# Kernel tuning notes

Hardware: AMD Instinct MI355X
Metric: run time of the kernel (lower is better)

## Reference

```python
import jax, jax.numpy as jnp
import numpy as np

D_MODEL = 1024
H = 16
D_K = D_MODEL // H


def setup_inputs() -> dict:
    key = jax.random.key(0)
    ks = jax.random.split(key, 7)
    B, S = 4, 2048
    scale = 1.0 / np.sqrt(D_MODEL)
    return {
        "q": jax.random.normal(ks[0], (B, S, D_MODEL), dtype=jnp.float32),
        "k": jax.random.normal(ks[1], (B, S, D_MODEL), dtype=jnp.float32),
        "v": jax.random.normal(ks[2], (B, S, D_MODEL), dtype=jnp.float32),
        "W_q": jax.random.normal(ks[3], (D_MODEL, D_MODEL), dtype=jnp.float32) * scale,
        "W_k": jax.random.normal(ks[4], (D_MODEL, D_MODEL), dtype=jnp.float32) * scale,
        "W_v": jax.random.normal(ks[5], (D_MODEL, D_MODEL), dtype=jnp.float32) * scale,
        "W_o": jax.random.normal(ks[6], (D_MODEL, D_MODEL), dtype=jnp.float32) * scale,
    }


def reference(q, k, v, W_q, W_k, W_v, W_o):
    B, S, _ = q.shape
    # nn.Linear(bias=False): y = x @ W.T
    def proj(x, W):
        return (x @ W.T).reshape(B, -1, H, D_K).transpose(0, 2, 1, 3)  # [B,H,S,d_k]
    Q = proj(q, W_q)
    K = proj(k, W_k)
    V = proj(v, W_v)
    scores = jnp.einsum('bhqd,bhkd->bhqk', Q, K) / jnp.sqrt(jnp.float32(D_K))
    attn = jax.nn.softmax(scores, axis=-1)  # dropout p=0.0 -> identity
    ctx = jnp.einsum('bhqk,bhkd->bhqd', attn, V)
    ctx = ctx.transpose(0, 2, 1, 3).reshape(B, S, H * D_K)
    return ctx @ W_o.T
```

## Files before the change

### kernel.cpp

```cpp
#include <hip/hip_runtime.h>
#include <stdint.h>


typedef __attribute__((ext_vector_type(8))) short bf16x8;
typedef __attribute__((ext_vector_type(4))) float f32x4;

__device__ __forceinline__ void lds_async16(const void* g, void* l) {
  __builtin_amdgcn_global_load_lds(
      (const __attribute__((address_space(1))) void*)g,
      (__attribute__((address_space(3))) void*)l, 16, 0, 0);
}

__device__ __forceinline__ unsigned short f2bf(float f) {
  union { float f; unsigned u; } v; v.f = f;
  unsigned u = v.u + 0x7fffu + ((v.u >> 16) & 1u);
  return (unsigned short)(u >> 16);
}

__device__ __forceinline__ float fast_exp2(float x) {
#if __has_builtin(__builtin_amdgcn_exp2f)
  return __builtin_amdgcn_exp2f(x);
#else
  return exp2f(x);
#endif
}

__device__ __forceinline__ unsigned pk2(float a, float b) {
#if __has_builtin(__builtin_amdgcn_cvt_pk_bf16_f32)
  typedef __bf16 bf16v2 __attribute__((ext_vector_type(2)));
  union { bf16v2 v; unsigned u; } x;
  x.v = __builtin_amdgcn_cvt_pk_bf16_f32(a, b);
  return x.u;
#else
  return (unsigned)f2bf(a) | ((unsigned)f2bf(b) << 16);
#endif
}

__global__ void cvt_kernel(const float* s0, const float* s1, const float* s2, const float* s3,
                           unsigned short* d0, unsigned short* d1, unsigned short* d2, unsigned short* d3,
                           int n4) {
  int which = blockIdx.y;
  const float* s = which == 0 ? s0 : which == 1 ? s1 : which == 2 ? s2 : s3;
  unsigned short* d = which == 0 ? d0 : which == 1 ? d1 : which == 2 ? d2 : d3;
  int i = blockIdx.x * 256 + threadIdx.x;
  if (i < n4) {
    float4 v = ((const float4*)s)[i];
    ushort4 o;
    o.x = f2bf(v.x); o.y = f2bf(v.y); o.z = f2bf(v.z); o.w = f2bf(v.w);
    ((ushort4*)d)[i] = o;
  }
}

struct GemmAcc { f32x4 acc[4][4]; };

__device__ __forceinline__ void gemm_core(const unsigned short* __restrict__ Arows,
                                          const unsigned short* __restrict__ Brows,
                                          int tm, int tn, unsigned short* As,
                                          unsigned short* Bs, GemmAcc& g) {
  constexpr int K = 1024;
  const int tid = threadIdx.x;
  const int lane = tid & 63;
  const int wv = tid >> 6;
  const int wm = wv & 1, wn = wv >> 1;
  const int c16 = lane & 15, q4 = lane >> 4;

#pragma unroll
  for (int i = 0; i < 4; ++i)
#pragma unroll
    for (int j = 0; j < 4; ++j)
#pragma unroll
      for (int r = 0; r < 4; ++r) g.acc[i][j][r] = 0.f;

  const int srow = tid >> 3;
  const int gc = (((tid & 7) ^ (srow & 7)) << 3);
  const unsigned short* Arow = Arows + (size_t)(tm * 128 + srow) * K + gc;
  const unsigned short* Brow = Brows + (size_t)(tn * 128 + srow) * K + gc;
  char* AsBase = (char*)As + tid * 16;
  char* BsBase = (char*)Bs + tid * 16;

  for (int k0 = 0; k0 < K; k0 += 64) {
    __syncthreads();
#pragma unroll
    for (int i = 0; i < 4; ++i) {
      lds_async16(Arow + k0 + i * 32 * K, AsBase + i * 4096);
      lds_async16(Brow + k0 + i * 32 * K, BsBase + i * 4096);
    }
    __syncthreads();
#pragma unroll
    for (int ks = 0; ks < 2; ++ks) {
      bf16x8 af[4], bfr[4];
#pragma unroll
      for (int i = 0; i < 4; ++i) {
        int mr = wm * 64 + i * 16 + c16;
        int pa = (ks * 4 + q4) ^ (mr & 7);
        af[i] = *(const bf16x8*)(As + mr * 64 + pa * 8);
        int nr = wn * 64 + i * 16 + c16;
        int pb = (ks * 4 + q4) ^ (nr & 7);
        bfr[i] = *(const bf16x8*)(Bs + nr * 64 + pb * 8);
      }
#pragma unroll
      for (int i = 0; i < 4; ++i)
#pragma unroll
        for (int j = 0; j < 4; ++j)
          g.acc[i][j] = __builtin_amdgcn_mfma_f32_16x16x32_bf16(af[i], bfr[j], g.acc[i][j], 0, 0, 0);
    }
  }
}

__global__ __launch_bounds__(256, 2)
void qkv_kernel(const unsigned short* __restrict__ qb, const unsigned short* __restrict__ kb,
                const unsigned short* __restrict__ vb,
                const unsigned short* __restrict__ wq, const unsigned short* __restrict__ wk,
                const unsigned short* __restrict__ wv_,
                unsigned short* __restrict__ Qb, unsigned short* __restrict__ Kb,
                unsigned short* __restrict__ Vtb) {
  __shared__ unsigned short As[128 * 64];
  __shared__ unsigned short Bs[128 * 64];
  const int z = blockIdx.z;
  const unsigned short* A;
  const unsigned short* B;
  int tm, tn;
  if (z == 0)      { A = qb;  B = wq;  tm = blockIdx.y; tn = blockIdx.x; }
  else if (z == 1) { A = kb;  B = wk;  tm = blockIdx.y; tn = blockIdx.x; }
  else             { A = wv_; B = vb;  tm = blockIdx.x; tn = blockIdx.y; }

  GemmAcc g;
  gemm_core(A, B, tm, tn, As, Bs, g);

  const int lane = threadIdx.x & 63;
  const int wv = threadIdx.x >> 6;
  const int wm = wv & 1, wn = wv >> 1;
  const int c16 = lane & 15, q4 = lane >> 4;
  const float qscale = 0.125f * 1.44269504f;

#pragma unroll
  for (int i = 0; i < 4; ++i)
#pragma unroll
    for (int j = 0; j < 4; ++j)
#pragma unroll
      for (int r = 0; r < 4; ++r) {
        int m = tm * 128 + wm * 64 + i * 16 + q4 * 4 + r;
        int n = tn * 128 + wn * 64 + j * 16 + c16;
        float val = g.acc[i][j][r];
        if (z < 2) {
          if (z == 0) val *= qscale;
          int b = m >> 11, s_ = m & 2047, h = n >> 6, d = n & 63;
          unsigned short* dst = z == 0 ? Qb : Kb;
          dst[(((size_t)(b * 16 + h) * 2048 + s_) << 6) | d] = f2bf(val);
        } else {
          int h = m >> 6, d = m & 63, b = n >> 11, s_ = n & 2047;
          int sl = s_ & 127;
          int sp = (sl & ~31) | (((sl >> 2) & 3) << 3) | (((sl >> 4) & 1) << 2) | (sl & 3);
          s_ = (s_ & ~127) | sp;
          Vtb[((size_t)((b * 16 + h) * 64 + d) << 11) | s_] = f2bf(val);
        }
      }
}

__global__ __launch_bounds__(256, 2)
void out_gemm(const unsigned short* __restrict__ A, const unsigned short* __restrict__ B,
              float* __restrict__ C) {
  __shared__ unsigned short As[128 * 64];
  __shared__ unsigned short Bs[128 * 64];
  GemmAcc g;
  gemm_core(A, B, blockIdx.y, blockIdx.x, As, Bs, g);
  const int lane = threadIdx.x & 63;
  const int wv = threadIdx.x >> 6;
  const int wm = wv & 1, wn = wv >> 1;
  const int c16 = lane & 15, q4 = lane >> 4;
#pragma unroll
  for (int i = 0; i < 4; ++i)
#pragma unroll
    for (int j = 0; j < 4; ++j)
#pragma unroll
      for (int r = 0; r < 4; ++r) {
        int m = blockIdx.y * 128 + wm * 64 + i * 16 + q4 * 4 + r;
        int n = blockIdx.x * 128 + wn * 64 + j * 16 + c16;
        C[(size_t)m * 1024 + n] = g.acc[i][j][r];
      }
}

__global__ __launch_bounds__(256, 2)
void attn_kernel(const unsigned short* __restrict__ Q,
                 const unsigned short* __restrict__ K,
                 const unsigned short* __restrict__ Vt,
                 unsigned short* __restrict__ ctx) {
  __shared__ unsigned short Ks[2][128 * 64];
  __shared__ unsigned short Vs[2][64 * 128];

  const int tid = threadIdx.x, lane = tid & 63, w = tid >> 6;
  const int c16 = lane & 15, q4 = lane >> 4;
  const int wbase = w * 64;
  const int bh = blockIdx.y, qt = blockIdx.x;
  const unsigned short* Qp = Q + ((size_t)bh * 2048 + qt * 256) * 64;
  const unsigned short* Kp = K + (size_t)bh * 2048 * 64;
  const unsigned short* Vp = Vt + (size_t)bh * 64 * 2048;

  const int srow8 = tid >> 3;
  const int gc8 = (((tid & 7) ^ (srow8 & 7)) << 3);

  {
    const unsigned short* Qr = Qp + (size_t)srow8 * 64 + gc8;
    char* base = (char*)Ks + tid * 16;
#pragma unroll
    for (int c = 0; c < 8; ++c) lds_async16(Qr + c * 32 * 64, base + c * 4096);
  }
  __syncthreads();
  const unsigned short* Kflat = &Ks[0][0];
  bf16x8 qf[4][2];
#pragma unroll
  for (int nn = 0; nn < 4; ++nn)
#pragma unroll
    for (int ks = 0; ks < 2; ++ks) {
      int qr = wbase + nn * 16 + c16;
      int pos = (ks * 4 + q4) ^ (qr & 7);
      qf[nn][ks] = *(const bf16x8*)(Kflat + qr * 64 + pos * 8);
    }
  __syncthreads();

  bf16x8 onesf;
  {
    short v = (c16 == 0) ? (short)0x3F80 : (short)0;
#pragma unroll
    for (int j = 0; j < 8; ++j) onesf[j] = v;
  }

  f32x4 oacc[4][4];
  f32x4 lacc[4];
#pragma unroll
  for (int nn = 0; nn < 4; ++nn) {
#pragma unroll
    for (int r = 0; r < 4; ++r) lacc[nn][r] = 0.f;
#pragma unroll
    for (int dj = 0; dj < 4; ++dj)
#pragma unroll
      for (int r = 0; r < 4; ++r) oacc[nn][dj][r] = 0.f;
  }

  const int vrow = tid >> 4;
  const int vslot = tid & 15;
  const int vchunk = vslot ^ (vrow & 15);
  const unsigned short* Kr0 = Kp + (size_t)srow8 * 64 + gc8;
  const unsigned short* Vr0 = Vp + (size_t)vrow * 2048 + vchunk * 8;

  {
    char* kb = (char*)Ks[0] + tid * 16;
    char* vb = (char*)Vs[0] + tid * 16;
#pragma unroll
    for (int c = 0; c < 4; ++c) {
      lds_async16(Kr0 + c * 32 * 64, kb + c * 4096);
      lds_async16(Vr0 + (size_t)c * 16 * 2048, vb + c * 4096);
    }
  }

  int cur = 0;
  for (int kt = 0; kt < 16; ++kt) {
    __syncthreads();
    if (kt < 15) {
      char* kb = (char*)Ks[cur ^ 1] + tid * 16;
      char* vb = (char*)Vs[cur ^ 1] + tid * 16;
      const unsigned short* Krn = Kr0 + (size_t)(kt + 1) * 128 * 64;
      const unsigned short* Vrn = Vr0 + (size_t)(kt + 1) * 128;
#pragma unroll
      for (int c = 0; c < 4; ++c) {
        lds_async16(Krn + c * 32 * 64, kb + c * 4096);
        lds_async16(Vrn + (size_t)c * 16 * 2048, vb + c * 4096);
      }
    }

    const unsigned short* KsC = Ks[cur];
    const unsigned short* VsC = Vs[cur];

#pragma unroll
    for (int ks2 = 0; ks2 < 4; ++ks2) {
      f32x4 s[2][4];
#pragma unroll
      for (int ms = 0; ms < 2; ++ms) {
        const int row = (ks2 * 2 + ms) * 16 + c16;
        const bf16x8 kf0 = *(const bf16x8*)(KsC + row * 64 + ((0 + q4) ^ (row & 7)) * 8);
        const bf16x8 kf1 = *(const bf16x8*)(KsC + row * 64 + ((4 + q4) ^ (row & 7)) * 8);
#pragma unroll
        for (int nn = 0; nn < 4; ++nn) {
          f32x4 z = {0.f, 0.f, 0.f, 0.f};
          z = __builtin_amdgcn_mfma_f32_16x16x32_bf16(kf0, qf[nn][0], z, 0, 0, 0);
          z = __builtin_amdgcn_mfma_f32_16x16x32_bf16(kf1, qf[nn][1], z, 0, 0, 0);
          s[ms][nn] = z;
        }
      }
      bf16x8 pfv[4];
#pragma unroll
      for (int nn = 0; nn < 4; ++nn) {
        union PU { unsigned u[4]; bf16x8 v; } pf;
        pf.u[0] = pk2(fast_exp2(s[0][nn][0]), fast_exp2(s[0][nn][1]));
        pf.u[1] = pk2(fast_exp2(s[0][nn][2]), fast_exp2(s[0][nn][3]));
        pf.u[2] = pk2(fast_exp2(s[1][nn][0]), fast_exp2(s[1][nn][1]));
        pf.u[3] = pk2(fast_exp2(s[1][nn][2]), fast_exp2(s[1][nn][3]));
        pfv[nn] = pf.v;
        lacc[nn] = __builtin_amdgcn_mfma_f32_16x16x32_bf16(pf.v, onesf, lacc[nn], 0, 0, 0);
      }
#pragma unroll
      for (int dj = 0; dj < 4; ++dj) {
        const int dr = dj * 16 + c16;
        const bf16x8 vf = *(const bf16x8*)(VsC + dr * 128 + (((ks2 * 4 + q4) ^ (dr & 15))) * 8);
#pragma unroll
        for (int nn = 0; nn < 4; ++nn)
          oacc[nn][dj] = __builtin_amdgcn_mfma_f32_16x16x32_bf16(pfv[nn], vf, oacc[nn][dj], 0, 0, 0);
      }
    }
    cur ^= 1;
  }

  int b = bh >> 4, h = bh & 15;
#pragma unroll
  for (int nn = 0; nn < 4; ++nn)
#pragma unroll
    for (int r = 0; r < 4; ++r) {
      float l = __shfl(lacc[nn][r], lane & 48, 64);
      float inv = 1.f / l;
      int s_ = qt * 256 + wbase + nn * 16 + q4 * 4 + r;
#pragma unroll
      for (int dj = 0; dj < 4; ++dj) {
        int d = dj * 16 + c16;
        ctx[((size_t)(b * 2048 + s_)) * 1024 + h * 64 + d] = f2bf(oacc[nn][dj][r] * inv);
      }
    }
}

extern "C" void kernel_launch(void* const* d_in, const int* in_sizes, int n_in,
                              void* d_out, int out_size, void* d_ws, size_t ws_size,
                              hipStream_t stream) {
  const float* q  = (const float*)d_in[0];
  const float* k  = (const float*)d_in[1];
  const float* v  = (const float*)d_in[2];
  const float* Wq = (const float*)d_in[3];
  const float* Wk = (const float*)d_in[4];
  const float* Wv = (const float*)d_in[5];
  const float* Wo = (const float*)d_in[6];

  char* ws = (char*)d_ws;
  unsigned short* qb  = (unsigned short*)(ws);
  unsigned short* kb  = (unsigned short*)(ws + (16u << 20));
  unsigned short* vb  = (unsigned short*)(ws + (32u << 20));
  unsigned short* wqb = (unsigned short*)(ws + (48u << 20));
  unsigned short* wkb = (unsigned short*)(ws + (50u << 20));
  unsigned short* wvb = (unsigned short*)(ws + (52u << 20));
  unsigned short* wob = (unsigned short*)(ws + (54u << 20));
  unsigned short* Qb  = (unsigned short*)(ws + (56u << 20));
  unsigned short* Kb  = (unsigned short*)(ws + (72u << 20));
  unsigned short* Vtb = (unsigned short*)(ws + (88u << 20));
  unsigned short* ctxb = qb;

  cvt_kernel<<<dim3(1024, 4), 256, 0, stream>>>(Wq, Wk, Wv, Wo, wqb, wkb, wvb, wob, 262144);
  cvt_kernel<<<dim3(8192, 3), 256, 0, stream>>>(q, k, v, q, qb, kb, vb, qb, 2097152);

  qkv_kernel<<<dim3(8, 64, 3), 256, 0, stream>>>(qb, kb, vb, wqb, wkb, wvb, Qb, Kb, Vtb);

  attn_kernel<<<dim3(8, 64), 256, 0, stream>>>(Qb, Kb, Vtb, ctxb);

  out_gemm<<<dim3(8, 64), 256, 0, stream>>>(ctxb, wob, (float*)d_out);
}
```

Before: 331.6 us.

## Shrink attention blocks to two waves with 64-key tiles, remapped grid and setprio

The attention kernel now runs 128-thread blocks over 128 query rows with 64-key K/V tiles, so it launches 1024 smaller workgroups on a 1D grid. The grid index is remapped so neighbouring workgroups handle different batch-heads. V fragment loads are hoisted ahead of the exp step, and s_setprio raises wave priority around the MFMA sections to encourage overlap between waves. The aim is more resident workgroups and better MFMA/VALU interleaving, at the cost of twice as many loop iterations and barriers, and K/V being loaded by twice as many blocks per head.

```diff
diff --git a/kernel.cpp b/kernel.cpp
--- a/kernel.cpp
+++ b/kernel.cpp
@@ -180,30 +180,32 @@
       }
 }
 
-__global__ __launch_bounds__(256, 2)
+__global__ __launch_bounds__(128, 2)
 void attn_kernel(const unsigned short* __restrict__ Q,
                  const unsigned short* __restrict__ K,
                  const unsigned short* __restrict__ Vt,
                  unsigned short* __restrict__ ctx) {
-  __shared__ unsigned short Ks[2][128 * 64];
-  __shared__ unsigned short Vs[2][64 * 128];
+  __shared__ unsigned short Ks[2][64 * 64];
+  __shared__ unsigned short Vs[2][64 * 64];
 
   const int tid = threadIdx.x, lane = tid & 63, w = tid >> 6;
   const int c16 = lane & 15, q4 = lane >> 4;
   const int wbase = w * 64;
-  const int bh = blockIdx.y, qt = blockIdx.x;
-  const unsigned short* Qp = Q + ((size_t)bh * 2048 + qt * 256) * 64;
+  const unsigned wgid = blockIdx.x;
+  const int bh = (int)((wgid & 7u) * 8 + ((wgid >> 3) & 7u));
+  const int qt = (int)(wgid >> 6);
+  const unsigned short* Qp = Q + ((size_t)bh * 2048 + qt * 128) * 64;
   const unsigned short* Kp = K + (size_t)bh * 2048 * 64;
   const unsigned short* Vp = Vt + (size_t)bh * 64 * 2048;
 
-  const int srow8 = tid >> 3;
-  const int gc8 = (((tid & 7) ^ (srow8 & 7)) << 3);
+  const int srow = tid >> 3;
+  const int gcol = (((tid & 7) ^ (srow & 7)) << 3);
 
   {
-    const unsigned short* Qr = Qp + (size_t)srow8 * 64 + gc8;
+    const unsigned short* Qr = Qp + (size_t)srow * 64 + gcol;
     char* base = (char*)Ks + tid * 16;
 #pragma unroll
-    for (int c = 0; c < 8; ++c) lds_async16(Qr + c * 32 * 64, base + c * 4096);
+    for (int c = 0; c < 8; ++c) lds_async16(Qr + c * 16 * 64, base + c * 2048);
   }
   __syncthreads();
   const unsigned short* Kflat = &Ks[0][0];
@@ -237,34 +239,31 @@
       for (int r = 0; r < 4; ++r) oacc[nn][dj][r] = 0.f;
   }
 
-  const int vrow = tid >> 4;
-  const int vslot = tid & 15;
-  const int vchunk = vslot ^ (vrow & 15);
-  const unsigned short* Kr0 = Kp + (size_t)srow8 * 64 + gc8;
-  const unsigned short* Vr0 = Vp + (size_t)vrow * 2048 + vchunk * 8;
+  const unsigned short* Kr0 = Kp + (size_t)srow * 64 + gcol;
+  const unsigned short* Vr0 = Vp + (size_t)srow * 2048 + gcol;
 
   {
     char* kb = (char*)Ks[0] + tid * 16;
     char* vb = (char*)Vs[0] + tid * 16;
 #pragma unroll
     for (int c = 0; c < 4; ++c) {
-      lds_async16(Kr0 + c * 32 * 64, kb + c * 4096);
-      lds_async16(Vr0 + (size_t)c * 16 * 2048, vb + c * 4096);
+      lds_async16(Kr0 + (size_t)c * 16 * 64, kb + c * 2048);
+      lds_async16(Vr0 + (size_t)c * 16 * 2048, vb + c * 2048);
     }
   }
 
   int cur = 0;
-  for (int kt = 0; kt < 16; ++kt) {
+  for (int kt = 0; kt < 32; ++kt) {
     __syncthreads();
-    if (kt < 15) {
+    if (kt < 31) {
       char* kb = (char*)Ks[cur ^ 1] + tid * 16;
       char* vb = (char*)Vs[cur ^ 1] + tid * 16;
-      const unsigned short* Krn = Kr0 + (size_t)(kt + 1) * 128 * 64;
-      const unsigned short* Vrn = Vr0 + (size_t)(kt + 1) * 128;
+      const unsigned short* Krn = Kr0 + (size_t)(kt + 1) * 64 * 64;
+      const unsigned short* Vrn = Vr0 + (size_t)(kt + 1) * 64;
 #pragma unroll
       for (int c = 0; c < 4; ++c) {
-        lds_async16(Krn + c * 32 * 64, kb + c * 4096);
-        lds_async16(Vrn + (size_t)c * 16 * 2048, vb + c * 4096);
+        lds_async16(Krn + (size_t)c * 16 * 64, kb + c * 2048);
+        lds_async16(Vrn + (size_t)c * 16 * 2048, vb + c * 2048);
       }
     }
 
@@ -272,8 +271,9 @@
     const unsigned short* VsC = Vs[cur];
 
 #pragma unroll
-    for (int ks2 = 0; ks2 < 4; ++ks2) {
+    for (int ks2 = 0; ks2 < 2; ++ks2) {
       f32x4 s[2][4];
+      __builtin_amdgcn_s_setprio(1);
 #pragma unroll
       for (int ms = 0; ms < 2; ++ms) {
         const int row = (ks2 * 2 + ms) * 16 + c16;
@@ -286,6 +286,13 @@
           z = __builtin_amdgcn_mfma_f32_16x16x32_bf16(kf1, qf[nn][1], z, 0, 0, 0);
           s[ms][nn] = z;
         }
+      }
+      __builtin_amdgcn_s_setprio(0);
+      bf16x8 vf[4];
+#pragma unroll
+      for (int dj = 0; dj < 4; ++dj) {
+        const int dr = dj * 16 + c16;
+        vf[dj] = *(const bf16x8*)(VsC + dr * 64 + (((ks2 * 4 + q4) ^ (dr & 7))) * 8);
       }
       bf16x8 pfv[4];
 #pragma unroll
@@ -296,16 +303,17 @@
         pf.u[2] = pk2(fast_exp2(s[1][nn][0]), fast_exp2(s[1][nn][1]));
         pf.u[3] = pk2(fast_exp2(s[1][nn][2]), fast_exp2(s[1][nn][3]));
         pfv[nn] = pf.v;
-        lacc[nn] = __builtin_amdgcn_mfma_f32_16x16x32_bf16(pf.v, onesf, lacc[nn], 0, 0, 0);
-      }
-#pragma unroll
-      for (int dj = 0; dj < 4; ++dj) {
-        const int dr = dj * 16 + c16;
-        const bf16x8 vf = *(const bf16x8*)(VsC + dr * 128 + (((ks2 * 4 + q4) ^ (dr & 15))) * 8);
+      }
+      __builtin_amdgcn_s_setprio(1);
+#pragma unroll
+      for (int nn = 0; nn < 4; ++nn)
+        lacc[nn] = __builtin_amdgcn_mfma_f32_16x16x32_bf16(pfv[nn], onesf, lacc[nn], 0, 0, 0);
+#pragma unroll
+      for (int dj = 0; dj < 4; ++dj)
 #pragma unroll
         for (int nn = 0; nn < 4; ++nn)
-          oacc[nn][dj] = __builtin_amdgcn_mfma_f32_16x16x32_bf16(pfv[nn], vf, oacc[nn][dj], 0, 0, 0);
-      }
+          oacc[nn][dj] = __builtin_amdgcn_mfma_f32_16x16x32_bf16(pfv[nn], vf[dj], oacc[nn][dj], 0, 0, 0);
+      __builtin_amdgcn_s_setprio(0);
     }
     cur ^= 1;
   }
@@ -317,7 +325,7 @@
     for (int r = 0; r < 4; ++r) {
       float l = __shfl(lacc[nn][r], lane & 48, 64);
       float inv = 1.f / l;
-      int s_ = qt * 256 + wbase + nn * 16 + q4 * 4 + r;
+      int s_ = qt * 128 + wbase + nn * 16 + q4 * 4 + r;
 #pragma unroll
       for (int dj = 0; dj < 4; ++dj) {
         int d = dj * 16 + c16;
@@ -355,7 +363,7 @@
 
   qkv_kernel<<<dim3(8, 64, 3), 256, 0, stream>>>(qb, kb, vb, wqb, wkb, wvb, Qb, Kb, Vtb);
 
-  attn_kernel<<<dim3(8, 64), 256, 0, stream>>>(Qb, Kb, Vtb, ctxb);
+  attn_kernel<<<dim3(1024), 128, 0, stream>>>(Qb, Kb, Vtb, ctxb);
 
   out_gemm<<<dim3(8, 64), 256, 0, stream>>>(ctxb, wob, (float*)d_out);
 }
```

Result: no change. 329.1 us (-0.7%).
